# Kernel optimization log

Hardware: AMD Instinct MI355X
Metric: run time of the kernel (lower is better)

Reference implementation:

```python
import jax, jax.numpy as jnp
import numpy as np

K = 36  # neighbors

def _gather(points, idx):
    # points: [B,N,C], idx: [B,N,K] -> [B,N,K,C]
    return jax.vmap(lambda p, i: p[i])(points, idx)

def setup_inputs() -> dict:
    key = jax.random.key(0)
    ks = jax.random.split(key, 16)
    B, N, d_points, d_model = 4, 4096, 32, 128
    def lin(k, fan_in, shape):
        return jax.random.normal(k, shape, dtype=jnp.float32) / np.sqrt(fan_in)
    return {
        "features": jax.random.normal(ks[0], (B, N, d_points), dtype=jnp.float32),
        "xyz": jax.random.uniform(ks[1], (B, N, 3), dtype=jnp.float32),
        "W1": lin(ks[2], d_points, (d_model, d_points)), "b1": jnp.zeros((d_model,), jnp.float32),
        "W2": lin(ks[3], d_model, (d_model, d_model)), "b2": jnp.zeros((d_model,), jnp.float32),
        "Wd1": lin(ks[4], 3, (d_model, 3)), "bd1": jnp.zeros((d_model,), jnp.float32),
        "Wd2": lin(ks[5], d_model, (d_model, d_model)), "bd2": jnp.zeros((d_model,), jnp.float32),
        "Wg1": lin(ks[6], d_model, (d_model, d_model)), "bg1": jnp.zeros((d_model,), jnp.float32),
        "Wg2": lin(ks[7], d_model, (d_model, d_model)), "bg2": jnp.zeros((d_model,), jnp.float32),
    }

def reference(features, xyz, W1, b1, W2, b2, Wd1, bd1, Wd2, bd2, Wg1, bg1, Wg2, bg2):
    # square_distance: [B,N,N]
    sq = jnp.sum(xyz * xyz, axis=-1)
    dists = sq[:, :, None] + sq[:, None, :] - 2.0 * jnp.einsum('bnc,bmc->bnm', xyz, xyz)
    knn_idx = jnp.argsort(dists, axis=-1)[:, :, :K]            # [B,N,K]
    knn_xyz = _gather(xyz, knn_idx)                             # [B,N,K,3]
    x = features @ W1.T + b1                                    # [B,N,d]
    k = _gather(x, knn_idx)                                     # [B,N,K,d]
    v = k
    # fc_delta(xyz[:,:,None] - knn_xyz)
    d_in = xyz[:, :, None, :] - knn_xyz                         # [B,N,K,3]
    pos_enc = jax.nn.relu(d_in @ Wd1.T + bd1) @ Wd2.T + bd2     # [B,N,K,d]
    # fc_gamma(q[:,:,None] - k + pos_enc)
    g_in = x[:, :, None, :] - k + pos_enc
    attn_pre = jax.nn.relu(g_in @ Wg1.T + bg1) @ Wg2.T + bg2    # [B,N,K,d]
    attn = jax.nn.softmax(attn_pre / np.sqrt(x.shape[-1]).astype(np.float32), axis=-2)
    res = jnp.einsum('bmnf,bmnf->bmf', attn, v + pos_enc)       # [B,N,d]
    res = res @ W2.T + b2 + x
    return (res, attn)
```

## Files before the change

kernel.cpp:

```cpp
#include <hip/hip_runtime.h>
#include <math.h>

#define BB 4
#define NPT 4096
#define DP 32
#define DD 128
#define KNB 36

typedef unsigned short ushort_t;
typedef unsigned int uint_t;
typedef unsigned long long ull;
typedef __attribute__((ext_vector_type(8))) short bf16x8;
typedef __attribute__((ext_vector_type(4))) float f32x4;
typedef __attribute__((ext_vector_type(4))) uint_t u32x4;

__device__ __forceinline__ ushort_t f2bf(float f) {
    unsigned u = __float_as_uint(f);
    unsigned r = (u + 0x7FFFu + ((u >> 16) & 1u)) >> 16;
    return (ushort_t)r;
}
__device__ __forceinline__ uint_t cvtpk(float lo, float hi) {
    uint_t r;
    asm("v_cvt_pk_bf16_f32 %0, %1, %2" : "=v"(r) : "v"(lo), "v"(hi));
    return r;
}
__device__ __forceinline__ ushort_t f2bf1(float f) { return (ushort_t)cvtpk(f, f); }
__device__ __forceinline__ float bf2f(ushort_t h) {
    return __uint_as_float((unsigned)h << 16);
}
__device__ __forceinline__ int swzi(int r, int f) {
    return (r << 7) + (((f >> 3) ^ (r & 15)) << 3) + (f & 7);
}

__global__ __launch_bounds__(256) void k_wcvt(const float* __restrict__ Wd2,
                                              const float* __restrict__ Wg1,
                                              const float* __restrict__ Wg2,
                                              const float* __restrict__ W2,
                                              ushort_t* __restrict__ wb) {
    int i = blockIdx.x * 256 + threadIdx.x;
    wb[i]           = f2bf(Wd2[i]);
    wb[i + 16384]   = f2bf(Wg1[i]);
    wb[i + 32768]   = f2bf(Wg2[i]);
    wb[i + 49152]   = f2bf(W2[i]);
}

__global__ __launch_bounds__(256) void k_x(const float* __restrict__ feat,
                                           const float* __restrict__ xyz,
                                           const float* __restrict__ W1,
                                           const float* __restrict__ b1,
                                           float* __restrict__ x,
                                           ushort_t* __restrict__ xb,
                                           float4* __restrict__ xyz4) {
    int g = threadIdx.x >> 7;
    int row = blockIdx.x * 2 + g;
    int t = threadIdx.x & 127;
    __shared__ float sf[2][DP];
    if (t < DP) sf[g][t] = feat[row * DP + t];
    __syncthreads();
    float acc = 0.f;
#pragma unroll
    for (int c = 0; c < DP; ++c) acc = fmaf(sf[g][c], W1[t * DP + c], acc);
    float xv = acc + b1[t];
    x[(size_t)row * DD + t] = xv;
    xb[(size_t)row * DD + t] = f2bf1(xv);
    if (t == 0) {
        float a = xyz[row * 3 + 0], b = xyz[row * 3 + 1], c = xyz[row * 3 + 2];
        float s = __fadd_rn(__fadd_rn(__fmul_rn(a, a), __fmul_rn(b, b)),
                            __fmul_rn(c, c));
        xyz4[row] = make_float4(a, b, c, s);
    }
}

__global__ __launch_bounds__(256) void k_knn2(const float4* __restrict__ xyz4,
                                              int* __restrict__ knn) {
    const int row = blockIdx.x;
    const int b = row >> 12;
    const int t = threadIdx.x;
    const int lane = t & 63, wv = t >> 6;

    __shared__ __align__(16) ull cand[2048];
    __shared__ int wsum[4];
    __shared__ ull wred[4];
    __shared__ ull sbest;
    __shared__ int sC, sCnt;

    uint_t* hist4 = (uint_t*)cand;

    const float4 q = xyz4[row];
    const float4* bp = xyz4 + (size_t)b * NPT;

#pragma unroll
    for (int i = 0; i < 16; ++i) hist4[t + (i << 8)] = 0;
    if (t == 0) sCnt = 0;
    __syncthreads();

    uint_t k16[16];
#pragma unroll
    for (int i = 0; i < 16; ++i) {
        int m = t + (i << 8);
        float4 p = bp[m];
        float d0 = __fmul_rn(q.x, p.x);
        float d1 = __fmaf_rn(q.y, p.y, d0);
        float dot = __fmaf_rn(q.z, p.z, d1);
        float d = __fsub_rn(__fadd_rn(q.w, p.w), __fmul_rn(2.0f, dot));
        unsigned u = __float_as_uint(d);
        u = (u & 0x80000000u) ? ~u : (u | 0x80000000u);
        k16[i] = u;
        int bin = (u < 0x80000000u) ? 0 : (int)((u - 0x80000000u) >> 21);
        atomicAdd(&hist4[(bin << 2) | (t & 3)], 1u);
    }
    __syncthreads();

    int s_t = 0;
#pragma unroll
    for (int i = 0; i < 16; ++i) s_t += (int)hist4[(t << 4) + i];
    int v = s_t;
    for (int off = 1; off < 64; off <<= 1) {
        int o = __shfl_up(v, off, 64);
        if (lane >= off) v += o;
    }
    if (lane == 63) wsum[wv] = v;
    __syncthreads();
    int base = 0;
    for (int w0 = 0; w0 < wv; ++w0) base += wsum[w0];
    int cumIncl = base + v, cumExcl = cumIncl - s_t;
    if (cumExcl < KNB && cumIncl >= KNB) {
        int run = cumExcl;
#pragma unroll
        for (int j = 0; j < 4; ++j) {
            int bb = (t << 2) + j;
            int h = (int)(hist4[(bb << 2) + 0] + hist4[(bb << 2) + 1] +
                          hist4[(bb << 2) + 2] + hist4[(bb << 2) + 3]);
            if (run + h >= KNB) { sC = bb; break; }
            run += h;
        }
    }
    __syncthreads();
    const int C = sC;

#pragma unroll
    for (int i = 0; i < 16; ++i) {
        uint_t u = k16[i];
        int bin = (u < 0x80000000u) ? 0 : (int)((u - 0x80000000u) >> 21);
        if (bin <= C) {
            int p = atomicAdd(&sCnt, 1);
            if (p < 2048) cand[p] = ((ull)u << 32) | (uint_t)(t + (i << 8));
        }
    }
    __syncthreads();
    const int cnt = sCnt;

    if (cnt <= 64) {
        if (wv == 0) {
            ull x = (lane < cnt) ? cand[lane] : ~0ull;
#pragma unroll
            for (int k = 2; k <= 64; k <<= 1) {
#pragma unroll
                for (int j = k >> 1; j > 0; j >>= 1) {
                    ull o = __shfl_xor(x, j, 64);
                    bool up = ((lane & k) == 0);
                    bool lower = ((lane & j) == 0);
                    ull mn = (x < o) ? x : o;
                    ull mx = (x < o) ? o : x;
                    x = (up == lower) ? mn : mx;
                }
            }
            if (lane < KNB) knn[(size_t)row * KNB + lane] = (int)(x & 0xffffffffu);
        }
        return;
    }

    if (cnt <= 2048) {
        ull lk = ~0ull;
        for (int i = t; i < cnt; i += 256) { ull k = cand[i]; if (k < lk) lk = k; }
        for (int r = 0; r < KNB; ++r) {
            ull k = lk;
#pragma unroll
            for (int off = 32; off >= 1; off >>= 1) {
                ull o = __shfl_down(k, off, 64);
                if (o < k) k = o;
            }
            if (lane == 0) wred[wv] = k;
            __syncthreads();
            if (t == 0) {
                ull best = wred[0];
                for (int w0 = 1; w0 < 4; ++w0) if (wred[w0] < best) best = wred[w0];
                sbest = best;
                knn[(size_t)row * KNB + r] = (int)(best & 0xffffffffu);
            }
            __syncthreads();
            ull best = sbest;
            if (lk == best) {
                for (int i = t; i < cnt; i += 256)
                    if (cand[i] == best) cand[i] = ~0ull;
                ull nm = ~0ull;
                for (int i = t; i < cnt; i += 256) { ull kk = cand[i]; if (kk < nm) nm = kk; }
                lk = nm;
            }
        }
        return;
    }

    {
        uint_t* bm = (uint_t*)cand;
        if (t < 128) bm[t] = 0;
        __syncthreads();
        ull lk = ~0ull;
#pragma unroll
        for (int i = 0; i < 16; ++i) {
            ull k = ((ull)k16[i] << 32) | (uint_t)(t + (i << 8));
            if (k < lk) lk = k;
        }
        for (int r = 0; r < KNB; ++r) {
            ull k = lk;
#pragma unroll
            for (int off = 32; off >= 1; off >>= 1) {
                ull o = __shfl_down(k, off, 64);
                if (o < k) k = o;
            }
            if (lane == 0) wred[wv] = k;
            __syncthreads();
            if (t == 0) {
                ull best = wred[0];
                for (int w0 = 1; w0 < 4; ++w0) if (wred[w0] < best) best = wred[w0];
                sbest = best;
                knn[(size_t)row * KNB + r] = (int)(best & 0xffffffffu);
            }
            __syncthreads();
            ull best = sbest;
            int bi = (int)(best & 0xffffffffu);
            if ((bi & 255) == t) {
                bm[bi >> 5] |= (1u << (bi & 31));
                ull nm = ~0ull;
#pragma unroll
                for (int i = 0; i < 16; ++i) {
                    int m = t + (i << 8);
                    if ((bm[m >> 5] >> (m & 31)) & 1u) continue;
                    ull kk = ((ull)k16[i] << 32) | (uint_t)m;
                    if (kk < nm) nm = kk;
                }
                lk = nm;
            }
        }
    }
}

__global__ __launch_bounds__(256) void k_fused2(
    const float* __restrict__ xyz, const float* __restrict__ x,
    const ushort_t* __restrict__ xb,
    const int* __restrict__ knn,
    const float* __restrict__ Wd1, const float* __restrict__ bd1,
    const float* __restrict__ bd2, const float* __restrict__ bg1,
    const float* __restrict__ bg2, const float* __restrict__ b2,
    const ushort_t* __restrict__ Wd2b, const ushort_t* __restrict__ Wg1b,
    const ushort_t* __restrict__ Wg2b, const ushort_t* __restrict__ W2b,
    float* __restrict__ out_res, float* __restrict__ out_attn) {

    const int p0 = blockIdx.x * 2;
    const int b = p0 >> 12;
    const int t = threadIdx.x;
    const int w = t >> 6;
    const int l = t & 63;
    const int q4 = l >> 4;

    __shared__ __align__(16) ushort_t Abuf[72 * 128];
    __shared__ __align__(16) ushort_t Vbuf[72 * 128];
    __shared__ int sidxb[72];
    __shared__ float dxb[72 * 3];
    __shared__ float Wd1s[384];
    __shared__ float bd1s[128];

    const int c0 = ((w * 2) << 4) + (l & 15);
    const int c1 = c0 + 16;
    float xn_r[2][2];
#pragma unroll
    for (int g = 0; g < 2; ++g) {
        xn_r[0][g] = x[(size_t)(p0 + g) * DD + c0];
        xn_r[1][g] = x[(size_t)(p0 + g) * DD + c1];
    }
    const float bd2_r[2] = {bd2[c0], bd2[c1]};
    const float bg1_r[2] = {bg1[c0], bg1[c1]};
    const float bg2_r[2] = {bg2[c0], bg2[c1]};
    const float b2_r[2]  = {b2[c0],  b2[c1]};

    if (t < 72) sidxb[t] = knn[(size_t)p0 * KNB + t];
    if (t >= 72 && t < 200) bd1s[t - 72] = bd1[t - 72];
    if (t >= 128 && t < 128 + 96) {
        int i = t - 128;
        reinterpret_cast<float4*>(Wd1s)[i] = reinterpret_cast<const float4*>(Wd1)[i];
    }
    __syncthreads();

    if (t < 72) {
        int g = (t >= KNB);
        int j = sidxb[t];
#pragma unroll
        for (int c = 0; c < 3; ++c)
            dxb[t * 3 + c] = xyz[(size_t)(p0 + g) * 3 + c] - xyz[((size_t)(b << 12) + j) * 3 + c];
    }
    for (int e = t; e < 72 * 16; e += 256) {
        int r = e >> 4, cb = e & 15;
        bf16x8 v = *reinterpret_cast<const bf16x8*>(
            xb + ((size_t)(b << 12) + sidxb[r]) * DD + (cb << 3));
        *reinterpret_cast<bf16x8*>(&Vbuf[(r << 7) + (cb << 3)]) = v;
    }
    __syncthreads();

    {
        const int cb = t & 15;
        float w0v[8], w1v[8], w2v[8], bv[8];
#pragma unroll
        for (int u = 0; u < 8; ++u) {
            int f = (cb << 3) + u;
            w0v[u] = Wd1s[f * 3 + 0];
            w1v[u] = Wd1s[f * 3 + 1];
            w2v[u] = Wd1s[f * 3 + 2];
            bv[u]  = bd1s[f];
        }
#pragma unroll
        for (int i = 0; i < 5; ++i) {
            int r = (t >> 4) + (i << 4);
            if (r < 72) {
                float dx0 = dxb[r * 3 + 0], dx1 = dxb[r * 3 + 1], dx2 = dxb[r * 3 + 2];
                float v[8];
#pragma unroll
                for (int u = 0; u < 8; ++u)
                    v[u] = fmaxf(fmaf(w0v[u], dx0, fmaf(w1v[u], dx1, w2v[u] * dx2)) + bv[u], 0.f);
                u32x4 pk = {cvtpk(v[0], v[1]), cvtpk(v[2], v[3]),
                            cvtpk(v[4], v[5]), cvtpk(v[6], v[7])};
                *reinterpret_cast<u32x4*>(&Abuf[(r << 7) + ((cb ^ (r & 15)) << 3)]) = pk;
            }
        }
    }
    __syncthreads();

    const f32x4 z4 = {0.f, 0.f, 0.f, 0.f};

    auto run_gemm = [&](const ushort_t* Wb, f32x4 acc[5][2]) {
        bf16x8 bfrag[2][4];
#pragma unroll
        for (int n2 = 0; n2 < 2; ++n2)
#pragma unroll
            for (int kt = 0; kt < 4; ++kt) {
                int f = ((w * 2 + n2) << 4) + (l & 15);
                int k = (kt << 5) + ((l >> 4) << 3);
                bfrag[n2][kt] = *reinterpret_cast<const bf16x8*>(Wb + f * 128 + k);
            }
        __builtin_amdgcn_s_setprio(1);
#pragma unroll
        for (int mt = 0; mt < 5; ++mt) {
#pragma unroll
            for (int kt = 0; kt < 4; ++kt) {
                int r = (mt << 4) + (l & 15);
                int cs = ((kt << 2) + (l >> 4)) ^ (l & 15);
                bf16x8 a = *reinterpret_cast<const bf16x8*>(&Abuf[(r << 7) + (cs << 3)]);
                acc[mt][0] = __builtin_amdgcn_mfma_f32_16x16x32_bf16(a, bfrag[0][kt], acc[mt][0], 0, 0, 0);
                acc[mt][1] = __builtin_amdgcn_mfma_f32_16x16x32_bf16(a, bfrag[1][kt], acc[mt][1], 0, 0, 0);
            }
        }
        __builtin_amdgcn_s_setprio(0);
    };

    {
        f32x4 acc[5][2];
#pragma unroll
        for (int mt = 0; mt < 5; ++mt) { acc[mt][0] = z4; acc[mt][1] = z4; }
        run_gemm(Wd2b, acc);
        __syncthreads();
#pragma unroll
        for (int mt = 0; mt < 5; ++mt) {
            int row0 = (mt << 4) + (q4 << 2);
            if (row0 < 72) {
                int g = (row0 >= KNB);
#pragma unroll
                for (int n2 = 0; n2 < 2; ++n2) {
                    int col = (n2 == 0) ? c0 : c1;
                    float xn_sel = xn_r[n2][g];
#pragma unroll
                    for (int rr = 0; rr < 4; ++rr) {
                        int row = row0 + rr;
                        int vs = (row << 7) + col;
                        float pe = acc[mt][n2][rr] + bd2_r[n2];
                        float xk = bf2f(Vbuf[vs]);
                        Vbuf[vs] = f2bf1(xk + pe);
                        float gin = (xn_sel - xk) + pe;
                        Abuf[swzi(row, col)] = f2bf1(gin);
                    }
                }
            }
        }
        __syncthreads();
    }

    {
        f32x4 acc[5][2];
#pragma unroll
        for (int mt = 0; mt < 5; ++mt) { acc[mt][0] = z4; acc[mt][1] = z4; }
        run_gemm(Wg1b, acc);
        __syncthreads();
#pragma unroll
        for (int mt = 0; mt < 5; ++mt) {
            int row0 = (mt << 4) + (q4 << 2);
            if (row0 < 72) {
#pragma unroll
                for (int n2 = 0; n2 < 2; ++n2) {
                    int col = (n2 == 0) ? c0 : c1;
#pragma unroll
                    for (int rr = 0; rr < 4; ++rr)
                        Abuf[swzi(row0 + rr, col)] = f2bf1(fmaxf(acc[mt][n2][rr] + bg1_r[n2], 0.f));
                }
            }
        }
        __syncthreads();
    }

    {
        f32x4 acc[5][2];
#pragma unroll
        for (int mt = 0; mt < 5; ++mt) { acc[mt][0] = z4; acc[mt][1] = z4; }
        run_gemm(Wg2b, acc);
        __syncthreads();
#pragma unroll
        for (int mt = 0; mt < 5; ++mt) {
            int row0 = (mt << 4) + (q4 << 2);
            if (row0 < 72) {
#pragma unroll
                for (int n2 = 0; n2 < 2; ++n2) {
                    int col = (n2 == 0) ? c0 : c1;
#pragma unroll
                    for (int rr = 0; rr < 4; ++rr)
                        Abuf[((row0 + rr) << 7) + col] = f2bf1(acc[mt][n2][rr] + bg2_r[n2]);
                }
            }
        }
        __syncthreads();
    }

    const float cexp = 0.12751744f;
    float ra;
    {
        int g = t >> 7, f = t & 127;
        const ushort_t* sbase = Abuf + (g * KNB << 7) + f;
        const ushort_t* vbase = Vbuf + (g * KNB << 7) + f;
        float p[KNB];
        float m = -__builtin_inff();
#pragma unroll
        for (int kk = 0; kk < KNB; ++kk) {
            p[kk] = bf2f(sbase[kk << 7]);
            m = fmaxf(m, p[kk]);
        }
        float mc = m * cexp;
        float sum = 0.f;
#pragma unroll
        for (int kk = 0; kk < KNB; ++kk) {
            float e_ = __builtin_amdgcn_exp2f(fmaf(p[kk], cexp, -mc));
            p[kk] = e_;
            sum += e_;
        }
        float inv = 1.f / sum;
        ra = 0.f;
        float* obase = out_attn + ((size_t)(p0 + g) * KNB) * DD + f;
#pragma unroll
        for (int kk = 0; kk < KNB; ++kk) {
            float a_ = p[kk] * inv;
            obase[(size_t)kk * DD] = a_;
            ra = fmaf(a_, bf2f(vbase[kk << 7]), ra);
        }
    }
    __syncthreads();
    {
        int g = t >> 7, f = t & 127;
        Abuf[swzi(g, f)] = f2bf1(ra);
    }
    __syncthreads();

    {
        f32x4 acc0 = z4, acc1 = z4;
#pragma unroll
        for (int kt = 0; kt < 4; ++kt) {
            int r = (l & 15);
            int cs = ((kt << 2) + (l >> 4)) ^ (l & 15);
            bf16x8 a = *reinterpret_cast<const bf16x8*>(&Abuf[(r << 7) + (cs << 3)]);
            int k = (kt << 5) + ((l >> 4) << 3);
            bf16x8 b0 = *reinterpret_cast<const bf16x8*>(W2b + c0 * 128 + k);
            bf16x8 b1 = *reinterpret_cast<const bf16x8*>(W2b + c1 * 128 + k);
            acc0 = __builtin_amdgcn_mfma_f32_16x16x32_bf16(a, b0, acc0, 0, 0, 0);
            acc1 = __builtin_amdgcn_mfma_f32_16x16x32_bf16(a, b1, acc1, 0, 0, 0);
        }
        if ((l >> 4) == 0) {
#pragma unroll
            for (int rr = 0; rr < 2; ++rr) {
                out_res[(size_t)(p0 + rr) * DD + c0] = acc0[rr] + b2_r[0] + xn_r[0][rr];
                out_res[(size_t)(p0 + rr) * DD + c1] = acc1[rr] + b2_r[1] + xn_r[1][rr];
            }
        }
    }
}

extern "C" void kernel_launch(void* const* d_in, const int* in_sizes, int n_in,
                              void* d_out, int out_size, void* d_ws, size_t ws_size,
                              hipStream_t stream) {
    const float* feat = (const float*)d_in[0];
    const float* xyz = (const float*)d_in[1];
    const float* W1 = (const float*)d_in[2];
    const float* b1 = (const float*)d_in[3];
    const float* W2 = (const float*)d_in[4];
    const float* b2 = (const float*)d_in[5];
    const float* Wd1 = (const float*)d_in[6];
    const float* bd1 = (const float*)d_in[7];
    const float* Wd2 = (const float*)d_in[8];
    const float* bd2 = (const float*)d_in[9];
    const float* Wg1 = (const float*)d_in[10];
    const float* bg1 = (const float*)d_in[11];
    const float* Wg2 = (const float*)d_in[12];
    const float* bg2 = (const float*)d_in[13];

    float* out = (float*)d_out;
    float* out_res = out;
    float* out_attn = out + (size_t)BB * NPT * DD;

    float* ws_x = (float*)d_ws;
    float4* xyz4 = (float4*)(ws_x + (size_t)BB * NPT * DD);
    int* ws_idx = (int*)(xyz4 + (size_t)BB * NPT);
    ushort_t* wb = (ushort_t*)(ws_idx + (size_t)BB * NPT * KNB);
    ushort_t* Wd2b = wb;
    ushort_t* Wg1b = wb + 16384;
    ushort_t* Wg2b = wb + 32768;
    ushort_t* W2b = wb + 49152;
    ushort_t* xb = wb + 65536;

    hipLaunchKernelGGL(k_wcvt, dim3(64), dim3(256), 0, stream, Wd2, Wg1, Wg2, W2, wb);
    hipLaunchKernelGGL(k_x, dim3(BB * NPT / 2), dim3(256), 0, stream,
                       feat, xyz, W1, b1, ws_x, xb, xyz4);
    hipLaunchKernelGGL(k_knn2, dim3(BB * NPT), dim3(256), 0, stream,
                       xyz4, ws_idx);
    hipLaunchKernelGGL(k_fused2, dim3(BB * NPT / 2), dim3(256), 0, stream,
                       xyz, ws_x, xb, ws_idx, Wd1, bd1, bd2, bg1, bg2, b2,
                       Wd2b, Wg1b, Wg2b, W2b, out_res, out_attn);
}
```

Baseline: 325.4 us.

## Fuse KNN selection into the attention kernel, dropping the index workspace

New measurement: 420.1 us. 1.29x slower.

```diff
diff --git a/kernel.cpp b/kernel.cpp
--- a/kernel.cpp
+++ b/kernel.cpp
@@ -71,184 +71,9 @@
     }
 }
 
-__global__ __launch_bounds__(256) void k_knn2(const float4* __restrict__ xyz4,
-                                              int* __restrict__ knn) {
-    const int row = blockIdx.x;
-    const int b = row >> 12;
-    const int t = threadIdx.x;
-    const int lane = t & 63, wv = t >> 6;
-
-    __shared__ __align__(16) ull cand[2048];
-    __shared__ int wsum[4];
-    __shared__ ull wred[4];
-    __shared__ ull sbest;
-    __shared__ int sC, sCnt;
-
-    uint_t* hist4 = (uint_t*)cand;
-
-    const float4 q = xyz4[row];
-    const float4* bp = xyz4 + (size_t)b * NPT;
-
-#pragma unroll
-    for (int i = 0; i < 16; ++i) hist4[t + (i << 8)] = 0;
-    if (t == 0) sCnt = 0;
-    __syncthreads();
-
-    uint_t k16[16];
-#pragma unroll
-    for (int i = 0; i < 16; ++i) {
-        int m = t + (i << 8);
-        float4 p = bp[m];
-        float d0 = __fmul_rn(q.x, p.x);
-        float d1 = __fmaf_rn(q.y, p.y, d0);
-        float dot = __fmaf_rn(q.z, p.z, d1);
-        float d = __fsub_rn(__fadd_rn(q.w, p.w), __fmul_rn(2.0f, dot));
-        unsigned u = __float_as_uint(d);
-        u = (u & 0x80000000u) ? ~u : (u | 0x80000000u);
-        k16[i] = u;
-        int bin = (u < 0x80000000u) ? 0 : (int)((u - 0x80000000u) >> 21);
-        atomicAdd(&hist4[(bin << 2) | (t & 3)], 1u);
-    }
-    __syncthreads();
-
-    int s_t = 0;
-#pragma unroll
-    for (int i = 0; i < 16; ++i) s_t += (int)hist4[(t << 4) + i];
-    int v = s_t;
-    for (int off = 1; off < 64; off <<= 1) {
-        int o = __shfl_up(v, off, 64);
-        if (lane >= off) v += o;
-    }
-    if (lane == 63) wsum[wv] = v;
-    __syncthreads();
-    int base = 0;
-    for (int w0 = 0; w0 < wv; ++w0) base += wsum[w0];
-    int cumIncl = base + v, cumExcl = cumIncl - s_t;
-    if (cumExcl < KNB && cumIncl >= KNB) {
-        int run = cumExcl;
-#pragma unroll
-        for (int j = 0; j < 4; ++j) {
-            int bb = (t << 2) + j;
-            int h = (int)(hist4[(bb << 2) + 0] + hist4[(bb << 2) + 1] +
-                          hist4[(bb << 2) + 2] + hist4[(bb << 2) + 3]);
-            if (run + h >= KNB) { sC = bb; break; }
-            run += h;
-        }
-    }
-    __syncthreads();
-    const int C = sC;
-
-#pragma unroll
-    for (int i = 0; i < 16; ++i) {
-        uint_t u = k16[i];
-        int bin = (u < 0x80000000u) ? 0 : (int)((u - 0x80000000u) >> 21);
-        if (bin <= C) {
-            int p = atomicAdd(&sCnt, 1);
-            if (p < 2048) cand[p] = ((ull)u << 32) | (uint_t)(t + (i << 8));
-        }
-    }
-    __syncthreads();
-    const int cnt = sCnt;
-
-    if (cnt <= 64) {
-        if (wv == 0) {
-            ull x = (lane < cnt) ? cand[lane] : ~0ull;
-#pragma unroll
-            for (int k = 2; k <= 64; k <<= 1) {
-#pragma unroll
-                for (int j = k >> 1; j > 0; j >>= 1) {
-                    ull o = __shfl_xor(x, j, 64);
-                    bool up = ((lane & k) == 0);
-                    bool lower = ((lane & j) == 0);
-                    ull mn = (x < o) ? x : o;
-                    ull mx = (x < o) ? o : x;
-                    x = (up == lower) ? mn : mx;
-                }
-            }
-            if (lane < KNB) knn[(size_t)row * KNB + lane] = (int)(x & 0xffffffffu);
-        }
-        return;
-    }
-
-    if (cnt <= 2048) {
-        ull lk = ~0ull;
-        for (int i = t; i < cnt; i += 256) { ull k = cand[i]; if (k < lk) lk = k; }
-        for (int r = 0; r < KNB; ++r) {
-            ull k = lk;
-#pragma unroll
-            for (int off = 32; off >= 1; off >>= 1) {
-                ull o = __shfl_down(k, off, 64);
-                if (o < k) k = o;
-            }
-            if (lane == 0) wred[wv] = k;
-            __syncthreads();
-            if (t == 0) {
-                ull best = wred[0];
-                for (int w0 = 1; w0 < 4; ++w0) if (wred[w0] < best) best = wred[w0];
-                sbest = best;
-                knn[(size_t)row * KNB + r] = (int)(best & 0xffffffffu);
-            }
-            __syncthreads();
-            ull best = sbest;
-            if (lk == best) {
-                for (int i = t; i < cnt; i += 256)
-                    if (cand[i] == best) cand[i] = ~0ull;
-                ull nm = ~0ull;
-                for (int i = t; i < cnt; i += 256) { ull kk = cand[i]; if (kk < nm) nm = kk; }
-                lk = nm;
-            }
-        }
-        return;
-    }
-
-    {
-        uint_t* bm = (uint_t*)cand;
-        if (t < 128) bm[t] = 0;
-        __syncthreads();
-        ull lk = ~0ull;
-#pragma unroll
-        for (int i = 0; i < 16; ++i) {
-            ull k = ((ull)k16[i] << 32) | (uint_t)(t + (i << 8));
-            if (k < lk) lk = k;
-        }
-        for (int r = 0; r < KNB; ++r) {
-            ull k = lk;
-#pragma unroll
-            for (int off = 32; off >= 1; off >>= 1) {
-                ull o = __shfl_down(k, off, 64);
-                if (o < k) k = o;
-            }
-            if (lane == 0) wred[wv] = k;
-            __syncthreads();
-            if (t == 0) {
-                ull best = wred[0];
-                for (int w0 = 1; w0 < 4; ++w0) if (wred[w0] < best) best = wred[w0];
-                sbest = best;
-                knn[(size_t)row * KNB + r] = (int)(best & 0xffffffffu);
-            }
-            __syncthreads();
-            ull best = sbest;
-            int bi = (int)(best & 0xffffffffu);
-            if ((bi & 255) == t) {
-                bm[bi >> 5] |= (1u << (bi & 31));
-                ull nm = ~0ull;
-#pragma unroll
-                for (int i = 0; i < 16; ++i) {
-                    int m = t + (i << 8);
-                    if ((bm[m >> 5] >> (m & 31)) & 1u) continue;
-                    ull kk = ((ull)k16[i] << 32) | (uint_t)m;
-                    if (kk < nm) nm = kk;
-                }
-                lk = nm;
-            }
-        }
-    }
-}
-
-__global__ __launch_bounds__(256) void k_fused2(
-    const float* __restrict__ xyz, const float* __restrict__ x,
+__global__ __launch_bounds__(256) void k_fused3(
+    const float4* __restrict__ xyz4, const float* __restrict__ x,
     const ushort_t* __restrict__ xb,
-    const int* __restrict__ knn,
     const float* __restrict__ Wd1, const float* __restrict__ bd1,
     const float* __restrict__ bd2, const float* __restrict__ bg1,
     const float* __restrict__ bg2, const float* __restrict__ b2,
@@ -269,6 +94,10 @@
     __shared__ float dxb[72 * 3];
     __shared__ float Wd1s[384];
     __shared__ float bd1s[128];
+    __shared__ int wsum[4];
+    __shared__ ull wred[4];
+    __shared__ ull sbest;
+    __shared__ int sC, sCnt;
 
     const int c0 = ((w * 2) << 4) + (l & 15);
     const int c1 = c0 + 16;
@@ -283,20 +112,180 @@
     const float bg2_r[2] = {bg2[c0], bg2[c1]};
     const float b2_r[2]  = {b2[c0],  b2[c1]};
 
-    if (t < 72) sidxb[t] = knn[(size_t)p0 * KNB + t];
-    if (t >= 72 && t < 200) bd1s[t - 72] = bd1[t - 72];
-    if (t >= 128 && t < 128 + 96) {
+    if (t < 128) bd1s[t] = bd1[t];
+    if (t >= 128 && t < 224) {
         int i = t - 128;
         reinterpret_cast<float4*>(Wd1s)[i] = reinterpret_cast<const float4*>(Wd1)[i];
     }
-    __syncthreads();
+
+    {
+        ull* cand = reinterpret_cast<ull*>(Abuf);
+        uint_t* hist4 = reinterpret_cast<uint_t*>(Abuf);
+        const float4* bp = xyz4 + (size_t)b * NPT;
+
+#pragma unroll 1
+        for (int gg = 0; gg < 2; ++gg) {
+            const float4 q = xyz4[p0 + gg];
+#pragma unroll
+            for (int i = 0; i < 16; ++i) hist4[t + (i << 8)] = 0;
+            if (t == 0) sCnt = 0;
+            __syncthreads();
+
+            uint_t k16[16];
+#pragma unroll
+            for (int i = 0; i < 16; ++i) {
+                int m = t + (i << 8);
+                float4 p = bp[m];
+                float d0 = __fmul_rn(q.x, p.x);
+                float d1 = __fmaf_rn(q.y, p.y, d0);
+                float dot = __fmaf_rn(q.z, p.z, d1);
+                float d = __fsub_rn(__fadd_rn(q.w, p.w), __fmul_rn(2.0f, dot));
+                unsigned u = __float_as_uint(d);
+                u = (u & 0x80000000u) ? ~u : (u | 0x80000000u);
+                k16[i] = u;
+                int bin = (u < 0x80000000u) ? 0 : (int)((u - 0x80000000u) >> 21);
+                atomicAdd(&hist4[(bin << 2) | (t & 3)], 1u);
+            }
+            __syncthreads();
+
+            int s_t = 0;
+#pragma unroll
+            for (int i = 0; i < 16; ++i) s_t += (int)hist4[(t << 4) + i];
+            int v = s_t;
+            for (int off = 1; off < 64; off <<= 1) {
+                int o = __shfl_up(v, off, 64);
+                if (l >= off) v += o;
+            }
+            if (l == 63) wsum[w] = v;
+            __syncthreads();
+            int base = 0;
+            for (int w0 = 0; w0 < w; ++w0) base += wsum[w0];
+            int cumIncl = base + v, cumExcl = cumIncl - s_t;
+            if (cumExcl < KNB && cumIncl >= KNB) {
+                int run = cumExcl;
+#pragma unroll
+                for (int j = 0; j < 4; ++j) {
+                    int bb = (t << 2) + j;
+                    int h = (int)(hist4[(bb << 2) + 0] + hist4[(bb << 2) + 1] +
+                                  hist4[(bb << 2) + 2] + hist4[(bb << 2) + 3]);
+                    if (run + h >= KNB) { sC = bb; break; }
+                    run += h;
+                }
+            }
+            __syncthreads();
+            const int C = sC;
+
+#pragma unroll
+            for (int i = 0; i < 16; ++i) {
+                uint_t u = k16[i];
+                int bin = (u < 0x80000000u) ? 0 : (int)((u - 0x80000000u) >> 21);
+                if (bin <= C) {
+                    int p = atomicAdd(&sCnt, 1);
+                    if (p < 2048) cand[p] = ((ull)u << 32) | (uint_t)(t + (i << 8));
+                }
+            }
+            __syncthreads();
+            const int cnt = sCnt;
+
+            if (cnt <= 64) {
+                if (w == 0) {
+                    ull xk_ = (l < cnt) ? cand[l] : ~0ull;
+#pragma unroll
+                    for (int k = 2; k <= 64; k <<= 1) {
+#pragma unroll
+                        for (int j = k >> 1; j > 0; j >>= 1) {
+                            ull o = __shfl_xor(xk_, j, 64);
+                            bool up = ((l & k) == 0);
+                            bool lower = ((l & j) == 0);
+                            ull mn = (xk_ < o) ? xk_ : o;
+                            ull mx = (xk_ < o) ? o : xk_;
+                            xk_ = (up == lower) ? mn : mx;
+                        }
+                    }
+                    if (l < KNB) sidxb[gg * KNB + l] = (int)(xk_ & 0xffffffffu);
+                }
+            } else if (cnt <= 2048) {
+                ull lk = ~0ull;
+                for (int i = t; i < cnt; i += 256) { ull k = cand[i]; if (k < lk) lk = k; }
+                for (int r = 0; r < KNB; ++r) {
+                    ull k = lk;
+#pragma unroll
+                    for (int off = 32; off >= 1; off >>= 1) {
+                        ull o = __shfl_down(k, off, 64);
+                        if (o < k) k = o;
+                    }
+                    if (l == 0) wred[w] = k;
+                    __syncthreads();
+                    if (t == 0) {
+                        ull best = wred[0];
+                        for (int w0 = 1; w0 < 4; ++w0) if (wred[w0] < best) best = wred[w0];
+                        sbest = best;
+                        sidxb[gg * KNB + r] = (int)(best & 0xffffffffu);
+                    }
+                    __syncthreads();
+                    ull best = sbest;
+                    if (lk == best) {
+                        for (int i = t; i < cnt; i += 256)
+                            if (cand[i] == best) cand[i] = ~0ull;
+                        ull nm = ~0ull;
+                        for (int i = t; i < cnt; i += 256) { ull kk = cand[i]; if (kk < nm) nm = kk; }
+                        lk = nm;
+                    }
+                }
+            } else {
+                uint_t* bm = (uint_t*)cand;
+                if (t < 128) bm[t] = 0;
+                __syncthreads();
+                ull lk = ~0ull;
+#pragma unroll
+                for (int i = 0; i < 16; ++i) {
+                    ull k = ((ull)k16[i] << 32) | (uint_t)(t + (i << 8));
+                    if (k < lk) lk = k;
+                }
+                for (int r = 0; r < KNB; ++r) {
+                    ull k = lk;
+#pragma unroll
+                    for (int off = 32; off >= 1; off >>= 1) {
+                        ull o = __shfl_down(k, off, 64);
+                        if (o < k) k = o;
+                    }
+                    if (l == 0) wred[w] = k;
+                    __syncthreads();
+                    if (t == 0) {
+                        ull best = wred[0];
+                        for (int w0 = 1; w0 < 4; ++w0) if (wred[w0] < best) best = wred[w0];
+                        sbest = best;
+                        sidxb[gg * KNB + r] = (int)(best & 0xffffffffu);
+                    }
+                    __syncthreads();
+                    ull best = sbest;
+                    int bi = (int)(best & 0xffffffffu);
+                    if ((bi & 255) == t) {
+                        bm[bi >> 5] |= (1u << (bi & 31));
+                        ull nm = ~0ull;
+#pragma unroll
+                        for (int i = 0; i < 16; ++i) {
+                            int m = t + (i << 8);
+                            if ((bm[m >> 5] >> (m & 31)) & 1u) continue;
+                            ull kk = ((ull)k16[i] << 32) | (uint_t)m;
+                            if (kk < nm) nm = kk;
+                        }
+                        lk = nm;
+                    }
+                }
+            }
+            __syncthreads();
+        }
+    }
+
 
     if (t < 72) {
         int g = (t >= KNB);
-        int j = sidxb[t];
-#pragma unroll
-        for (int c = 0; c < 3; ++c)
-            dxb[t * 3 + c] = xyz[(size_t)(p0 + g) * 3 + c] - xyz[((size_t)(b << 12) + j) * 3 + c];
+        float4 pq = xyz4[p0 + g];
+        float4 pj = xyz4[(size_t)(b << 12) + sidxb[t]];
+        dxb[t * 3 + 0] = pq.x - pj.x;
+        dxb[t * 3 + 1] = pq.y - pj.y;
+        dxb[t * 3 + 2] = pq.z - pj.z;
     }
     for (int e = t; e < 72 * 16; e += 256) {
         int r = e >> 4, cb = e & 15;
@@ -521,8 +510,7 @@
 
     float* ws_x = (float*)d_ws;
     float4* xyz4 = (float4*)(ws_x + (size_t)BB * NPT * DD);
-    int* ws_idx = (int*)(xyz4 + (size_t)BB * NPT);
-    ushort_t* wb = (ushort_t*)(ws_idx + (size_t)BB * NPT * KNB);
+    ushort_t* wb = (ushort_t*)(xyz4 + (size_t)BB * NPT);
     ushort_t* Wd2b = wb;
     ushort_t* Wg1b = wb + 16384;
     ushort_t* Wg2b = wb + 32768;
@@ -532,9 +520,7 @@
     hipLaunchKernelGGL(k_wcvt, dim3(64), dim3(256), 0, stream, Wd2, Wg1, Wg2, W2, wb);
     hipLaunchKernelGGL(k_x, dim3(BB * NPT / 2), dim3(256), 0, stream,
                        feat, xyz, W1, b1, ws_x, xb, xyz4);
-    hipLaunchKernelGGL(k_knn2, dim3(BB * NPT), dim3(256), 0, stream,
-                       xyz4, ws_idx);
-    hipLaunchKernelGGL(k_fused2, dim3(BB * NPT / 2), dim3(256), 0, stream,
-                       xyz, ws_x, xb, ws_idx, Wd1, bd1, bd2, bg1, bg2, b2,
+    hipLaunchKernelGGL(k_fused3, dim3(BB * NPT / 2), dim3(256), 0, stream,
+                       xyz4, ws_x, xb, Wd1, bd1, bd2, bg1, bg2, b2,
                        Wd2b, Wg1b, Wg2b, W2b, out_res, out_attn);
 }
```

## Fold x projection into kNN kernel and xyz4 prep into weight conversion

Applied to the files above, without the earlier changes.

Result: faster. 317.2 us (-2.5%).

```diff
diff --git a/kernel.cpp b/kernel.cpp
--- a/kernel.cpp
+++ b/kernel.cpp
@@ -36,42 +36,31 @@
                                               const float* __restrict__ Wg1,
                                               const float* __restrict__ Wg2,
                                               const float* __restrict__ W2,
-                                              ushort_t* __restrict__ wb) {
-    int i = blockIdx.x * 256 + threadIdx.x;
-    wb[i]           = f2bf(Wd2[i]);
-    wb[i + 16384]   = f2bf(Wg1[i]);
-    wb[i + 32768]   = f2bf(Wg2[i]);
-    wb[i + 49152]   = f2bf(W2[i]);
-}
-
-__global__ __launch_bounds__(256) void k_x(const float* __restrict__ feat,
-                                           const float* __restrict__ xyz,
-                                           const float* __restrict__ W1,
-                                           const float* __restrict__ b1,
-                                           float* __restrict__ x,
-                                           ushort_t* __restrict__ xb,
-                                           float4* __restrict__ xyz4) {
-    int g = threadIdx.x >> 7;
-    int row = blockIdx.x * 2 + g;
-    int t = threadIdx.x & 127;
-    __shared__ float sf[2][DP];
-    if (t < DP) sf[g][t] = feat[row * DP + t];
-    __syncthreads();
-    float acc = 0.f;
-#pragma unroll
-    for (int c = 0; c < DP; ++c) acc = fmaf(sf[g][c], W1[t * DP + c], acc);
-    float xv = acc + b1[t];
-    x[(size_t)row * DD + t] = xv;
-    xb[(size_t)row * DD + t] = f2bf1(xv);
-    if (t == 0) {
-        float a = xyz[row * 3 + 0], b = xyz[row * 3 + 1], c = xyz[row * 3 + 2];
+                                              const float* __restrict__ xyz,
+                                              ushort_t* __restrict__ wb,
+                                              float4* __restrict__ xyz4) {
+    int t = threadIdx.x;
+    if (blockIdx.x < 64) {
+        int i = blockIdx.x * 256 + t;
+        wb[i]           = f2bf(Wd2[i]);
+        wb[i + 16384]   = f2bf(Wg1[i]);
+        wb[i + 32768]   = f2bf(Wg2[i]);
+        wb[i + 49152]   = f2bf(W2[i]);
+    } else {
+        int idx = (blockIdx.x - 64) * 256 + t;
+        float a = xyz[idx * 3 + 0], b = xyz[idx * 3 + 1], c = xyz[idx * 3 + 2];
         float s = __fadd_rn(__fadd_rn(__fmul_rn(a, a), __fmul_rn(b, b)),
                             __fmul_rn(c, c));
-        xyz4[row] = make_float4(a, b, c, s);
+        xyz4[idx] = make_float4(a, b, c, s);
     }
 }
 
 __global__ __launch_bounds__(256) void k_knn2(const float4* __restrict__ xyz4,
+                                              const float* __restrict__ feat,
+                                              const float* __restrict__ W1,
+                                              const float* __restrict__ b1,
+                                              float* __restrict__ x,
+                                              ushort_t* __restrict__ xb,
                                               int* __restrict__ knn) {
     const int row = blockIdx.x;
     const int b = row >> 12;
@@ -79,6 +68,7 @@
     const int lane = t & 63, wv = t >> 6;
 
     __shared__ __align__(16) ull cand[2048];
+    __shared__ float sf[DP];
     __shared__ int wsum[4];
     __shared__ ull wred[4];
     __shared__ ull sbest;
@@ -89,10 +79,20 @@
     const float4 q = xyz4[row];
     const float4* bp = xyz4 + (size_t)b * NPT;
 
+    if (t < DP) sf[t] = feat[row * DP + t];
 #pragma unroll
     for (int i = 0; i < 16; ++i) hist4[t + (i << 8)] = 0;
     if (t == 0) sCnt = 0;
     __syncthreads();
+
+    if (t < 128) {
+        float acc = 0.f;
+#pragma unroll
+        for (int c = 0; c < DP; ++c) acc = fmaf(sf[c], W1[t * DP + c], acc);
+        float xv = acc + b1[t];
+        x[(size_t)row * DD + t] = xv;
+        xb[(size_t)row * DD + t] = f2bf1(xv);
+    }
 
     uint_t k16[16];
 #pragma unroll
@@ -136,13 +136,12 @@
         }
     }
     __syncthreads();
-    const int C = sC;
+    const ull thr = 0x80000000ull + ((ull)(sC + 1) << 21);
 
 #pragma unroll
     for (int i = 0; i < 16; ++i) {
         uint_t u = k16[i];
-        int bin = (u < 0x80000000u) ? 0 : (int)((u - 0x80000000u) >> 21);
-        if (bin <= C) {
+        if ((ull)u < thr) {
             int p = atomicAdd(&sCnt, 1);
             if (p < 2048) cand[p] = ((ull)u << 32) | (uint_t)(t + (i << 8));
         }
@@ -152,20 +151,20 @@
 
     if (cnt <= 64) {
         if (wv == 0) {
-            ull x = (lane < cnt) ? cand[lane] : ~0ull;
+            ull x_ = (lane < cnt) ? cand[lane] : ~0ull;
 #pragma unroll
             for (int k = 2; k <= 64; k <<= 1) {
 #pragma unroll
                 for (int j = k >> 1; j > 0; j >>= 1) {
-                    ull o = __shfl_xor(x, j, 64);
+                    ull o = __shfl_xor(x_, j, 64);
                     bool up = ((lane & k) == 0);
                     bool lower = ((lane & j) == 0);
-                    ull mn = (x < o) ? x : o;
-                    ull mx = (x < o) ? o : x;
-                    x = (up == lower) ? mn : mx;
+                    ull mn = (x_ < o) ? x_ : o;
+                    ull mx = (x_ < o) ? o : x_;
+                    x_ = (up == lower) ? mn : mx;
                 }
             }
-            if (lane < KNB) knn[(size_t)row * KNB + lane] = (int)(x & 0xffffffffu);
+            if (lane < KNB) knn[(size_t)row * KNB + lane] = (int)(x_ & 0xffffffffu);
         }
         return;
     }
@@ -246,7 +245,7 @@
 }
 
 __global__ __launch_bounds__(256) void k_fused2(
-    const float* __restrict__ xyz, const float* __restrict__ x,
+    const float4* __restrict__ xyz4, const float* __restrict__ x,
     const ushort_t* __restrict__ xb,
     const int* __restrict__ knn,
     const float* __restrict__ Wd1, const float* __restrict__ bd1,
@@ -285,7 +284,7 @@
 
     if (t < 72) sidxb[t] = knn[(size_t)p0 * KNB + t];
     if (t >= 72 && t < 200) bd1s[t - 72] = bd1[t - 72];
-    if (t >= 128 && t < 128 + 96) {
+    if (t >= 128 && t < 224) {
         int i = t - 128;
         reinterpret_cast<float4*>(Wd1s)[i] = reinterpret_cast<const float4*>(Wd1)[i];
     }
@@ -293,10 +292,11 @@
 
     if (t < 72) {
         int g = (t >= KNB);
-        int j = sidxb[t];
-#pragma unroll
-        for (int c = 0; c < 3; ++c)
-            dxb[t * 3 + c] = xyz[(size_t)(p0 + g) * 3 + c] - xyz[((size_t)(b << 12) + j) * 3 + c];
+        float4 pq = xyz4[p0 + g];
+        float4 pj = xyz4[(size_t)(b << 12) + sidxb[t]];
+        dxb[t * 3 + 0] = pq.x - pj.x;
+        dxb[t * 3 + 1] = pq.y - pj.y;
+        dxb[t * 3 + 2] = pq.z - pj.z;
     }
     for (int e = t; e < 72 * 16; e += 256) {
         int r = e >> 4, cb = e & 15;
@@ -529,12 +529,11 @@
     ushort_t* W2b = wb + 49152;
     ushort_t* xb = wb + 65536;
 
-    hipLaunchKernelGGL(k_wcvt, dim3(64), dim3(256), 0, stream, Wd2, Wg1, Wg2, W2, wb);
-    hipLaunchKernelGGL(k_x, dim3(BB * NPT / 2), dim3(256), 0, stream,
-                       feat, xyz, W1, b1, ws_x, xb, xyz4);
+    hipLaunchKernelGGL(k_wcvt, dim3(128), dim3(256), 0, stream,
+                       Wd2, Wg1, Wg2, W2, xyz, wb, xyz4);
     hipLaunchKernelGGL(k_knn2, dim3(BB * NPT), dim3(256), 0, stream,
-                       xyz4, ws_idx);
+                       xyz4, feat, W1, b1, ws_x, xb, ws_idx);
     hipLaunchKernelGGL(k_fused2, dim3(BB * NPT / 2), dim3(256), 0, stream,
-                       xyz, ws_x, xb, ws_idx, Wd1, bd1, bd2, bg1, bg2, b2,
+                       xyz4, ws_x, xb, ws_idx, Wd1, bd1, bd2, bg1, bg2, b2,
                        Wd2b, Wg1b, Wg2b, W2b, out_res, out_attn);
 }
```
